# Optimization experiments

Measured on AMD Instinct MI355X. Metric: run time of the kernel, lower is better.

Reference implementation:

```python
import jax, jax.numpy as jnp
import numpy as np
from jax.ops import segment_sum

N = 100000
E = 1600000
NFEAT, NHID, NCLS = 128, 64, 40


def setup_inputs() -> dict:
    key = jax.random.key(0)
    ks = jax.random.split(key, 8)
    x = jax.random.normal(ks[0], (N, NFEAT), dtype=jnp.float32)
    edge_index = jax.random.randint(ks[1], (2, E), 0, N, dtype=jnp.int64)
    s = lambda fi, fo: (2.0 / (fi + fo)) ** 0.5  # glorot-ish
    W1 = jax.random.normal(ks[2], (NFEAT, NHID), dtype=jnp.float32) * s(NFEAT, NHID)
    b1 = jnp.zeros((NHID,), dtype=jnp.float32)
    W2 = jax.random.normal(ks[3], (NHID, NHID), dtype=jnp.float32) * s(NHID, NHID)
    b2 = jnp.zeros((NHID,), dtype=jnp.float32)
    Wc = jax.random.normal(ks[4], (NHID, NCLS), dtype=jnp.float32) * s(NHID, NCLS)
    bc = jnp.zeros((NCLS,), dtype=jnp.float32)
    return {"x": x, "edge_index": edge_index, "W1": W1, "b1": b1,
            "W2": W2, "b2": b2, "Wc": Wc, "bc": bc}


def _gcn_conv(x, W, b, row, col, dinv):
    # x: [N, Fin] -> [N, Fout]; symmetric-normalized aggregation (PyG GCNConv)
    h = x @ W                                   # [N, Fout]
    norm = dinv[row] * dinv[col]                # [E+N]
    msg = h[row] * norm[:, None]                # [E+N, Fout]
    out = segment_sum(msg, col, num_segments=N) # [N, Fout]
    return out + b


def reference(x, edge_index, W1, b1, W2, b2, Wc, bc):
    # add self loops
    loops = jnp.arange(N, dtype=edge_index.dtype)
    row = jnp.concatenate([edge_index[0], loops])
    col = jnp.concatenate([edge_index[1], loops])
    # symmetric normalization degrees (edge weight = 1)
    deg = segment_sum(jnp.ones_like(col, dtype=x.dtype), col, num_segments=N)
    dinv = jnp.where(deg > 0, jax.lax.rsqrt(deg), 0.0)
    h = jax.nn.relu(_gcn_conv(x, W1, b1, row, col, dinv))
    h = jax.nn.relu(_gcn_conv(h, W2, b2, row, col, dinv))
    return h @ Wc + bc
```

## Files before the change

### kernel.cpp

```cpp
#include <hip/hip_runtime.h>

#define NN 100000
#define NE 1600000
#define NF 128
#define NH 64
#define NC 40

#define BKN 128
#define NBK ((NN + BKN - 1) / BKN)
#define CH  4096
#define NCHB ((NE + CH - 1) / CH)
#define CAPB 2560
#define OFFS (BKN + 1)
#define HCAP 1408
#define HTS 36
#define XTS 68

typedef short bf16x8 __attribute__((ext_vector_type(8)));
typedef float f32x4  __attribute__((ext_vector_type(4)));

__device__ __forceinline__ unsigned short f2bf(float f) {
    unsigned int u = __builtin_bit_cast(unsigned int, f);
    u += 0x7FFFu + ((u >> 16) & 1u);
    return (unsigned short)(u >> 16);
}
__device__ __forceinline__ float bfl(unsigned int u) {
    return __builtin_bit_cast(float, u << 16);
}
__device__ __forceinline__ float bfh(unsigned int u) {
    return __builtin_bit_cast(float, u & 0xFFFF0000u);
}
__device__ __forceinline__ unsigned int pk2(float a, float b) {
    return (unsigned int)f2bf(a) | ((unsigned int)f2bf(b) << 16);
}
__device__ __forceinline__ void bacc8(float4& lo, float4& hi, uint4 v) {
    lo.x += bfl(v.x); hi.x += bfh(v.x);
    lo.y += bfl(v.y); hi.y += bfh(v.y);
    lo.z += bfl(v.z); hi.z += bfh(v.z);
    lo.w += bfl(v.w); hi.w += bfh(v.w);
}

__global__ __launch_bounds__(256) void prep_wt(const float* __restrict__ W1,
                                               const float* __restrict__ W2,
                                               const float* __restrict__ Wc,
                                               unsigned short* __restrict__ Wt1,
                                               unsigned short* __restrict__ Wt2,
                                               unsigned short* __restrict__ Wtc,
                                               int* __restrict__ gcnt) {
    int t = blockIdx.x * 256 + threadIdx.x;
    if (t < 8192) {
        int j = t >> 7, k = t & 127;
        Wt1[j * 128 + k] = f2bf(W1[k * 64 + j]);
    } else if (t < 8192 + 4096) {
        int u = t - 8192;
        int j = u >> 6, k = u & 63;
        Wt2[j * 64 + k] = f2bf(W2[k * 64 + j]);
    } else if (t < 8192 + 4096 + 3072) {
        int u = t - 8192 - 4096;
        int j = u >> 6, k = u & 63;
        Wtc[j * 64 + k] = (j < NC) ? f2bf(Wc[k * NC + j]) : (unsigned short)0;
    } else if (t < 8192 + 4096 + 3072 + NBK) {
        gcnt[t - 8192 - 4096 - 3072] = 0;
    }
}

__global__ __launch_bounds__(256) void bucket_scatter(const int* __restrict__ row,
                                                      const int* __restrict__ col,
                                                      int* __restrict__ gcnt,
                                                      unsigned int* __restrict__ encs) {
    __shared__ int h[NBK];
    __shared__ int loff[NBK];
    __shared__ int cur[NBK];
    __shared__ int gbase[NBK];
    __shared__ unsigned int stage[CH];
    __shared__ unsigned short sbkt[CH];
    int tid = threadIdx.x;
    for (int i = tid; i < NBK; i += 256) h[i] = 0;
    __syncthreads();
    int e0 = blockIdx.x * CH;
    int nval = NE - e0; if (nval > CH) nval = CH;
    int c[16];
    #pragma unroll
    for (int i = 0; i < 16; ++i) {
        int e = e0 + i * 256 + tid;
        c[i] = (e < NE) ? col[e] : -1;
        if (c[i] >= 0) atomicAdd(&h[c[i] >> 7], 1);
    }
    __syncthreads();
    if (tid < 64) {
        int lane = tid, base = lane * 13;
        int pre[13]; int sum = 0;
        #pragma unroll
        for (int j = 0; j < 13; ++j) {
            int idx = base + j;
            int x = (idx < NBK) ? h[idx] : 0;
            pre[j] = sum; sum += x;
        }
        int run = sum;
        #pragma unroll
        for (int d = 1; d < 64; d <<= 1) {
            int n = __shfl_up(run, d, 64);
            if (lane >= d) run += n;
        }
        int lex = run - sum;
        #pragma unroll
        for (int j = 0; j < 13; ++j) {
            int idx = base + j;
            if (idx < NBK) { loff[idx] = lex + pre[j]; cur[idx] = lex + pre[j]; }
        }
    }
    __syncthreads();
    for (int i = tid; i < NBK; i += 256) {
        int cnt = h[i];
        gbase[i] = cnt ? atomicAdd(&gcnt[i], cnt) : 0;
    }
    __syncthreads();
    #pragma unroll
    for (int i = 0; i < 16; ++i) {
        int e = e0 + i * 256 + tid;
        if (e < NE) {
            int cc = c[i], b = cc >> 7;
            int r = atomicAdd(&cur[b], 1);
            stage[r] = ((unsigned int)(cc & 127) << 24) | (unsigned int)row[e];
            sbkt[r] = (unsigned short)b;
        }
    }
    __syncthreads();
    for (int s = tid; s < nval; s += 256) {
        int b = sbkt[s];
        encs[(size_t)b * CAPB + gbase[b] + (s - loff[b])] = stage[s];
    }
}

__global__ __launch_bounds__(256) void csr_sort(unsigned int* __restrict__ encs,
                                                const int* __restrict__ gcnt,
                                                int* __restrict__ offg,
                                                float* __restrict__ dinv) {
    __shared__ unsigned int sseg[CAPB];
    __shared__ int h[BKN];
    __shared__ int off[OFFS];
    __shared__ int cur[BKN];
    int b = blockIdx.x, tid = threadIdx.x;
    if (tid < BKN) h[tid] = 0;
    __syncthreads();
    int m = gcnt[b];
    unsigned int* seg = encs + (size_t)b * CAPB;
    for (int s = tid; s < m; s += 256) {
        unsigned int e = seg[s];
        sseg[s] = e;
        atomicAdd(&h[e >> 24], 1);
    }
    __syncthreads();
    if (tid < BKN) {
        int g = b * BKN + tid;
        if (g < NN) dinv[g] = rsqrtf((float)(h[tid] + 1));
    }
    if (tid < 64) {
        int lane = tid;
        int x0 = h[lane * 2], x1 = h[lane * 2 + 1];
        int sum = x0 + x1, run = sum;
        #pragma unroll
        for (int d = 1; d < 64; d <<= 1) {
            int n = __shfl_up(run, d, 64);
            if (lane >= d) run += n;
        }
        int ex = run - sum;
        off[lane * 2] = ex;          cur[lane * 2] = ex;
        off[lane * 2 + 1] = ex + x0; cur[lane * 2 + 1] = ex + x0;
        if (lane == 63) off[BKN] = run;
    }
    __syncthreads();
    for (int s = tid; s < m; s += 256) {
        unsigned int e = sseg[s];
        int n = e >> 24;
        int r = atomicAdd(&cur[n], 1);
        seg[r] = e & 0xFFFFFFu;
    }
    if (tid < OFFS) offg[b * OFFS + tid] = off[tid];
}

__global__ __launch_bounds__(256) void gemm1_mfma(const float* __restrict__ x,
                                                  const unsigned short* __restrict__ Wt1,
                                                  const float* __restrict__ dinv,
                                                  unsigned short* __restrict__ hsb) {
    __shared__ unsigned int Xl[64 * XTS];
    __shared__ float sdv[64];
    int tid = threadIdx.x;
    int rbase = blockIdx.x * 64;
    if (tid < 64) {
        int r = rbase + tid;
        sdv[tid] = (r < NN) ? dinv[r] : 0.f;
    }
    #pragma unroll
    for (int p = 0; p < 8; ++p) {
        int fid = p * 256 + tid;
        int m = fid >> 5, c4 = fid & 31;
        int rr = rbase + m; if (rr >= NN) rr = NN - 1;
        float4 v = *(const float4*)(x + (size_t)rr * NF + c4 * 4);
        uint2 u;
        u.x = pk2(v.x, v.y);
        u.y = pk2(v.z, v.w);
        *(uint2*)&Xl[m * XTS + c4 * 2] = u;
    }
    __syncthreads();

    int wid = tid >> 6, lane = tid & 63;
    int lm = lane & 15, lg = lane >> 4;
    int rt = wid;
    bf16x8 af[4];
    #pragma unroll
    for (int kh = 0; kh < 4; ++kh)
        af[kh] = __builtin_bit_cast(bf16x8,
                    *(const uint4*)&Xl[(rt * 16 + lm) * XTS + kh * 16 + lg * 4]);
    f32x4 acc[4];
    #pragma unroll
    for (int ct = 0; ct < 4; ++ct) {
        acc[ct] = (f32x4){0.f, 0.f, 0.f, 0.f};
        #pragma unroll
        for (int kh = 0; kh < 4; ++kh) {
            bf16x8 bf = __builtin_bit_cast(bf16x8,
                *(const uint4*)(Wt1 + (size_t)(ct * 16 + lm) * 128 + kh * 32 + lg * 8));
            acc[ct] = __builtin_amdgcn_mfma_f32_16x16x32_bf16(af[kh], bf, acc[ct], 0, 0, 0);
        }
    }
    #pragma unroll
    for (int ct = 0; ct < 4; ++ct) {
        #pragma unroll
        for (int rg = 0; rg < 4; ++rg) {
            int rloc = rt * 16 + lg * 4 + rg;
            int r = rbase + rloc;
            if (r < NN)
                hsb[(size_t)r * NH + ct * 16 + lm] = f2bf(acc[ct][rg] * sdv[rloc]);
        }
    }
}

template <int FINAL>
__global__ __launch_bounds__(512) void agg_matmul(const unsigned short* __restrict__ hs,
                                                  const int* __restrict__ srow,
                                                  const int* __restrict__ offg,
                                                  const float* __restrict__ dinv,
                                                  const float* __restrict__ biasA,
                                                  const unsigned short* __restrict__ Wt,
                                                  const float* __restrict__ biasB,
                                                  unsigned short* __restrict__ hsb_out,
                                                  float* __restrict__ f_out) {
    __shared__ int off[65];
    __shared__ int sidx[HCAP];
    __shared__ unsigned int htb[64 * HTS];
    __shared__ float sdinv[64];
    int b = blockIdx.x >> 1, half = blockIdx.x & 1;
    int tid = threadIdx.x;
    int rbase = b * BKN + half * 64;
    if (tid < 65) off[tid] = offg[b * OFFS + half * 64 + tid];
    __syncthreads();
    int e0 = off[0], cnt = off[64] - e0;
    const int* ptr = srow + (size_t)b * CAPB + e0;
    for (int s = tid; s < cnt; s += 512) sidx[s] = ptr[s];
    __syncthreads();

    int n = tid >> 3, sl = tid & 7;
    int g = rbase + n;
    const uint4* hs8 = (const uint4*)hs;
    {
        float d = (g < NN) ? dinv[g] : 0.f;
        if (sl == 0) sdinv[n] = d;
        float4 o0 = {}, o1 = {};
        if (g < NN) {
            float4 lo0 = {}, hi0 = {}, lo1 = {}, hi1 = {};
            float4 lo2 = {}, hi2 = {}, lo3 = {}, hi3 = {};
            bacc8(lo0, hi0, hs8[(size_t)g * 8 + sl]);
            int e = off[n] - e0, ee = off[n + 1] - e0;
            for (; e + 8 <= ee; e += 8) {
                int r0 = sidx[e + 0], r1 = sidx[e + 1];
                int r2 = sidx[e + 2], r3 = sidx[e + 3];
                int r4 = sidx[e + 4], r5 = sidx[e + 5];
                int r6 = sidx[e + 6], r7 = sidx[e + 7];
                uint4 v0 = hs8[(size_t)r0 * 8 + sl];
                uint4 v1 = hs8[(size_t)r1 * 8 + sl];
                uint4 v2 = hs8[(size_t)r2 * 8 + sl];
                uint4 v3 = hs8[(size_t)r3 * 8 + sl];
                uint4 v4 = hs8[(size_t)r4 * 8 + sl];
                uint4 v5 = hs8[(size_t)r5 * 8 + sl];
                uint4 v6 = hs8[(size_t)r6 * 8 + sl];
                uint4 v7 = hs8[(size_t)r7 * 8 + sl];
                bacc8(lo0, hi0, v0); bacc8(lo1, hi1, v1);
                bacc8(lo2, hi2, v2); bacc8(lo3, hi3, v3);
                bacc8(lo0, hi0, v4); bacc8(lo1, hi1, v5);
                bacc8(lo2, hi2, v6); bacc8(lo3, hi3, v7);
            }
            if (e + 4 <= ee) {
                int r0 = sidx[e + 0], r1 = sidx[e + 1];
                int r2 = sidx[e + 2], r3 = sidx[e + 3];
                uint4 v0 = hs8[(size_t)r0 * 8 + sl];
                uint4 v1 = hs8[(size_t)r1 * 8 + sl];
                uint4 v2 = hs8[(size_t)r2 * 8 + sl];
                uint4 v3 = hs8[(size_t)r3 * 8 + sl];
                bacc8(lo0, hi0, v0); bacc8(lo1, hi1, v1);
                bacc8(lo2, hi2, v2); bacc8(lo3, hi3, v3);
                e += 4;
            }
            for (; e < ee; ++e)
                bacc8(lo0, hi0, hs8[(size_t)sidx[e] * 8 + sl]);
            lo0.x += lo1.x + lo2.x + lo3.x;  hi0.x += hi1.x + hi2.x + hi3.x;
            lo0.y += lo1.y + lo2.y + lo3.y;  hi0.y += hi1.y + hi2.y + hi3.y;
            lo0.z += lo1.z + lo2.z + lo3.z;  hi0.z += hi1.z + hi2.z + hi3.z;
            lo0.w += lo1.w + lo2.w + lo3.w;  hi0.w += hi1.w + hi2.w + hi3.w;
            float4 bb0 = ((const float4*)biasA)[sl * 2];
            float4 bb1 = ((const float4*)biasA)[sl * 2 + 1];
            o0.x = fmaxf(fmaf(lo0.x, d, bb0.x), 0.f);
            o0.y = fmaxf(fmaf(hi0.x, d, bb0.y), 0.f);
            o0.z = fmaxf(fmaf(lo0.y, d, bb0.z), 0.f);
            o0.w = fmaxf(fmaf(hi0.y, d, bb0.w), 0.f);
            o1.x = fmaxf(fmaf(lo0.z, d, bb1.x), 0.f);
            o1.y = fmaxf(fmaf(hi0.z, d, bb1.y), 0.f);
            o1.z = fmaxf(fmaf(lo0.w, d, bb1.z), 0.f);
            o1.w = fmaxf(fmaf(hi0.w, d, bb1.w), 0.f);
        }
        uint4 pk;
        pk.x = pk2(o0.x, o0.y);
        pk.y = pk2(o0.z, o0.w);
        pk.z = pk2(o1.x, o1.y);
        pk.w = pk2(o1.z, o1.w);
        *(uint4*)&htb[n * HTS + sl * 4] = pk;
    }
    __syncthreads();

    constexpr int NCT = FINAL ? 3 : 4;
    int wid = tid >> 6, lane = tid & 63;
    int lm = lane & 15, lg = lane >> 4;
    int rt = wid >> 1;
    int ct0 = (wid & 1) * 2;
    int ct1 = (ct0 + 2 < NCT) ? ct0 + 2 : NCT;
    bf16x8 afrag[2];
    #pragma unroll
    for (int kh = 0; kh < 2; ++kh) {
        const unsigned int* p = &htb[(rt * 16 + lm) * HTS + kh * 16 + lg * 4];
        afrag[kh] = __builtin_bit_cast(bf16x8, *(const uint4*)p);
    }
    for (int ct = ct0; ct < ct1; ++ct) {
        f32x4 acc = (f32x4){0.f, 0.f, 0.f, 0.f};
        #pragma unroll
        for (int kh = 0; kh < 2; ++kh) {
            const unsigned short* q = Wt + (size_t)(ct * 16 + lm) * 64 + kh * 32 + lg * 8;
            bf16x8 bfrag = __builtin_bit_cast(bf16x8, *(const uint4*)q);
            acc = __builtin_amdgcn_mfma_f32_16x16x32_bf16(afrag[kh], bfrag, acc, 0, 0, 0);
        }
        if (!FINAL) {
            #pragma unroll
            for (int rg = 0; rg < 4; ++rg) {
                int rloc = rt * 16 + lg * 4 + rg;
                int r = rbase + rloc;
                if (r < NN) {
                    float v = acc[rg] * sdinv[rloc];
                    hsb_out[(size_t)r * NH + ct * 16 + lm] = f2bf(v);
                }
            }
        } else {
            int c = ct * 16 + lm;
            if (c < NC) {
                float bb = biasB[c];
                #pragma unroll
                for (int rg = 0; rg < 4; ++rg) {
                    int rloc = rt * 16 + lg * 4 + rg;
                    int r = rbase + rloc;
                    if (r < NN)
                        f_out[(size_t)r * NC + c] = acc[rg] + bb;
                }
            }
        }
    }
}


extern "C" void kernel_launch(void* const* d_in, const int* in_sizes, int n_in,
                              void* d_out, int out_size, void* d_ws, size_t ws_size,
                              hipStream_t stream) {
    const float* x  = (const float*)d_in[0];
    const int* ei   = (const int*)d_in[1];
    const int* row  = ei;
    const int* col  = ei + NE;
    const float* W1 = (const float*)d_in[2];
    const float* b1 = (const float*)d_in[3];
    const float* W2 = (const float*)d_in[4];
    const float* b2 = (const float*)d_in[5];
    const float* Wc = (const float*)d_in[6];
    const float* bc = (const float*)d_in[7];
    float* out = (float*)d_out;

    char* ws = (char*)d_ws;
    size_t off = 0;
    auto alloc = [&](size_t bytes) {
        void* p = ws + off;
        off = (off + bytes + 255) & ~(size_t)255;
        return p;
    };
    int*   gcnt = (int*)alloc((size_t)NBK * 4);
    int*   offg = (int*)alloc((size_t)NBK * OFFS * 4);
    float* dinv = (float*)alloc((size_t)NN * 4);
    unsigned int* encs = (unsigned int*)alloc((size_t)NBK * CAPB * 4);
    unsigned short* hsb1 = (unsigned short*)alloc((size_t)NN * NH * 2);
    unsigned short* hsb2 = (unsigned short*)alloc((size_t)NN * NH * 2);
    unsigned short* Wt1  = (unsigned short*)alloc((size_t)64 * 128 * 2);
    unsigned short* Wt2  = (unsigned short*)alloc((size_t)64 * 64 * 2);
    unsigned short* Wtc  = (unsigned short*)alloc((size_t)48 * 64 * 2);

    const int GB = (NN + 63) / 64;

    prep_wt<<<64, 256, 0, stream>>>(W1, W2, Wc, Wt1, Wt2, Wtc, gcnt);
    bucket_scatter<<<NCHB, 256, 0, stream>>>(row, col, gcnt, encs);
    csr_sort<<<NBK, 256, 0, stream>>>(encs, gcnt, offg, dinv);

    gemm1_mfma<<<GB, 256, 0, stream>>>(x, Wt1, dinv, hsb1);
    agg_matmul<0><<<NBK * 2, 512, 0, stream>>>(hsb1, (const int*)encs, offg, dinv,
                                               b1, Wt2, nullptr, hsb2, nullptr);
    agg_matmul<1><<<NBK * 2, 512, 0, stream>>>(hsb2, (const int*)encs, offg, dinv,
                                               b2, Wtc, bc, nullptr, out);
}
```

Baseline: 151.3 us.

## Split features into plane-major slices with XCC-aware dynamic block scheduling

Hidden activations are stored as 8 feature planes of 8 bf16 values each. Aggregation is split per (bucket, plane), and blocks take work from atomic counters keyed by their XCC ID, so each XCC's L2 tends to serve one plane's gather working set. The fused aggregate+matmul kernels are split into a separate aggregation kernel and a plane-reading MFMA GEMM, which adds two launches and extra intermediate round-trips through memory. Each edge gather now fetches only 16 bytes, so there are more, smaller requests, in exchange for a smaller per-XCC L2 footprint.

```diff
diff --git a/kernel.cpp b/kernel.cpp
--- a/kernel.cpp
+++ b/kernel.cpp
@@ -12,8 +12,6 @@
 #define NCHB ((NE + CH - 1) / CH)
 #define CAPB 2560
 #define OFFS (BKN + 1)
-#define HCAP 1408
-#define HTS 36
 #define XTS 68
 
 typedef short bf16x8 __attribute__((ext_vector_type(8)));
@@ -33,11 +31,9 @@
 __device__ __forceinline__ unsigned int pk2(float a, float b) {
     return (unsigned int)f2bf(a) | ((unsigned int)f2bf(b) << 16);
 }
-__device__ __forceinline__ void bacc8(float4& lo, float4& hi, uint4 v) {
-    lo.x += bfl(v.x); hi.x += bfh(v.x);
-    lo.y += bfl(v.y); hi.y += bfh(v.y);
-    lo.z += bfl(v.z); hi.z += bfh(v.z);
-    lo.w += bfl(v.w); hi.w += bfh(v.w);
+__device__ __forceinline__ void add4(float4& a, uint2 v) {
+    a.x += bfl(v.x); a.y += bfh(v.x);
+    a.z += bfl(v.y); a.w += bfh(v.y);
 }
 
 __global__ __launch_bounds__(256) void prep_wt(const float* __restrict__ W1,
@@ -46,7 +42,8 @@
                                                unsigned short* __restrict__ Wt1,
                                                unsigned short* __restrict__ Wt2,
                                                unsigned short* __restrict__ Wtc,
-                                               int* __restrict__ gcnt) {
+                                               int* __restrict__ gcnt,
+                                               int* __restrict__ curs) {
     int t = blockIdx.x * 256 + threadIdx.x;
     if (t < 8192) {
         int j = t >> 7, k = t & 127;
@@ -59,8 +56,10 @@
         int u = t - 8192 - 4096;
         int j = u >> 6, k = u & 63;
         Wtc[j * 64 + k] = (j < NC) ? f2bf(Wc[k * NC + j]) : (unsigned short)0;
-    } else if (t < 8192 + 4096 + 3072 + NBK) {
-        gcnt[t - 8192 - 4096 - 3072] = 0;
+    } else if (t < 15360 + NBK) {
+        gcnt[t - 15360] = 0;
+    } else if (t < 15360 + NBK + 16) {
+        curs[t - 15360 - NBK] = 0;
     }
 }
 
@@ -182,7 +181,7 @@
 __global__ __launch_bounds__(256) void gemm1_mfma(const float* __restrict__ x,
                                                   const unsigned short* __restrict__ Wt1,
                                                   const float* __restrict__ dinv,
-                                                  unsigned short* __restrict__ hsb) {
+                                                  uint4* __restrict__ hsbT) {
     __shared__ unsigned int Xl[64 * XTS];
     __shared__ float sdv[64];
     int tid = threadIdx.x;
@@ -206,12 +205,11 @@
 
     int wid = tid >> 6, lane = tid & 63;
     int lm = lane & 15, lg = lane >> 4;
-    int rt = wid;
     bf16x8 af[4];
     #pragma unroll
     for (int kh = 0; kh < 4; ++kh)
         af[kh] = __builtin_bit_cast(bf16x8,
-                    *(const uint4*)&Xl[(rt * 16 + lm) * XTS + kh * 16 + lg * 4]);
+                    *(const uint4*)&Xl[(wid * 16 + lm) * XTS + kh * 16 + lg * 4]);
     f32x4 acc[4];
     #pragma unroll
     for (int ct = 0; ct < 4; ++ct) {
@@ -223,153 +221,156 @@
             acc[ct] = __builtin_amdgcn_mfma_f32_16x16x32_bf16(af[kh], bf, acc[ct], 0, 0, 0);
         }
     }
-    #pragma unroll
-    for (int ct = 0; ct < 4; ++ct) {
+    __syncthreads();
+    unsigned short* ot = (unsigned short*)Xl;
+    #pragma unroll
+    for (int ct = 0; ct < 4; ++ct)
         #pragma unroll
         for (int rg = 0; rg < 4; ++rg) {
-            int rloc = rt * 16 + lg * 4 + rg;
-            int r = rbase + rloc;
-            if (r < NN)
-                hsb[(size_t)r * NH + ct * 16 + lm] = f2bf(acc[ct][rg] * sdv[rloc]);
-        }
+            int rloc = wid * 16 + lg * 4 + rg;
+            ot[rloc * 72 + ct * 16 + lm] = f2bf(acc[ct][rg] * sdv[rloc]);
+        }
+    __syncthreads();
+    unsigned int* otU = (unsigned int*)Xl;
+    for (int j = tid; j < 512; j += 256) {
+        int p = j >> 6, i = j & 63;
+        int r = rbase + i;
+        if (r < NN)
+            hsbT[(size_t)p * NN + r] = *(uint4*)&otU[i * 36 + p * 4];
     }
 }
 
 template <int FINAL>
-__global__ __launch_bounds__(512) void agg_matmul(const unsigned short* __restrict__ hs,
-                                                  const int* __restrict__ srow,
-                                                  const int* __restrict__ offg,
-                                                  const float* __restrict__ dinv,
-                                                  const float* __restrict__ biasA,
-                                                  const unsigned short* __restrict__ Wt,
-                                                  const float* __restrict__ biasB,
-                                                  unsigned short* __restrict__ hsb_out,
-                                                  float* __restrict__ f_out) {
-    __shared__ int off[65];
-    __shared__ int sidx[HCAP];
-    __shared__ unsigned int htb[64 * HTS];
-    __shared__ float sdinv[64];
-    int b = blockIdx.x >> 1, half = blockIdx.x & 1;
-    int tid = threadIdx.x;
-    int rbase = b * BKN + half * 64;
-    if (tid < 65) off[tid] = offg[b * OFFS + half * 64 + tid];
-    __syncthreads();
-    int e0 = off[0], cnt = off[64] - e0;
-    const int* ptr = srow + (size_t)b * CAPB + e0;
-    for (int s = tid; s < cnt; s += 512) sidx[s] = ptr[s];
-    __syncthreads();
-
-    int n = tid >> 3, sl = tid & 7;
-    int g = rbase + n;
-    const uint4* hs8 = (const uint4*)hs;
-    {
-        float d = (g < NN) ? dinv[g] : 0.f;
-        if (sl == 0) sdinv[n] = d;
-        float4 o0 = {}, o1 = {};
-        if (g < NN) {
-            float4 lo0 = {}, hi0 = {}, lo1 = {}, hi1 = {};
-            float4 lo2 = {}, hi2 = {}, lo3 = {}, hi3 = {};
-            bacc8(lo0, hi0, hs8[(size_t)g * 8 + sl]);
-            int e = off[n] - e0, ee = off[n + 1] - e0;
-            for (; e + 8 <= ee; e += 8) {
-                int r0 = sidx[e + 0], r1 = sidx[e + 1];
-                int r2 = sidx[e + 2], r3 = sidx[e + 3];
-                int r4 = sidx[e + 4], r5 = sidx[e + 5];
-                int r6 = sidx[e + 6], r7 = sidx[e + 7];
-                uint4 v0 = hs8[(size_t)r0 * 8 + sl];
-                uint4 v1 = hs8[(size_t)r1 * 8 + sl];
-                uint4 v2 = hs8[(size_t)r2 * 8 + sl];
-                uint4 v3 = hs8[(size_t)r3 * 8 + sl];
-                uint4 v4 = hs8[(size_t)r4 * 8 + sl];
-                uint4 v5 = hs8[(size_t)r5 * 8 + sl];
-                uint4 v6 = hs8[(size_t)r6 * 8 + sl];
-                uint4 v7 = hs8[(size_t)r7 * 8 + sl];
-                bacc8(lo0, hi0, v0); bacc8(lo1, hi1, v1);
-                bacc8(lo2, hi2, v2); bacc8(lo3, hi3, v3);
-                bacc8(lo0, hi0, v4); bacc8(lo1, hi1, v5);
-                bacc8(lo2, hi2, v6); bacc8(lo3, hi3, v7);
-            }
-            if (e + 4 <= ee) {
-                int r0 = sidx[e + 0], r1 = sidx[e + 1];
-                int r2 = sidx[e + 2], r3 = sidx[e + 3];
-                uint4 v0 = hs8[(size_t)r0 * 8 + sl];
-                uint4 v1 = hs8[(size_t)r1 * 8 + sl];
-                uint4 v2 = hs8[(size_t)r2 * 8 + sl];
-                uint4 v3 = hs8[(size_t)r3 * 8 + sl];
-                bacc8(lo0, hi0, v0); bacc8(lo1, hi1, v1);
-                bacc8(lo2, hi2, v2); bacc8(lo3, hi3, v3);
-                e += 4;
-            }
-            for (; e < ee; ++e)
-                bacc8(lo0, hi0, hs8[(size_t)sidx[e] * 8 + sl]);
-            lo0.x += lo1.x + lo2.x + lo3.x;  hi0.x += hi1.x + hi2.x + hi3.x;
-            lo0.y += lo1.y + lo2.y + lo3.y;  hi0.y += hi1.y + hi2.y + hi3.y;
-            lo0.z += lo1.z + lo2.z + lo3.z;  hi0.z += hi1.z + hi2.z + hi3.z;
-            lo0.w += lo1.w + lo2.w + lo3.w;  hi0.w += hi1.w + hi2.w + hi3.w;
-            float4 bb0 = ((const float4*)biasA)[sl * 2];
-            float4 bb1 = ((const float4*)biasA)[sl * 2 + 1];
-            o0.x = fmaxf(fmaf(lo0.x, d, bb0.x), 0.f);
-            o0.y = fmaxf(fmaf(hi0.x, d, bb0.y), 0.f);
-            o0.z = fmaxf(fmaf(lo0.y, d, bb0.z), 0.f);
-            o0.w = fmaxf(fmaf(hi0.y, d, bb0.w), 0.f);
-            o1.x = fmaxf(fmaf(lo0.z, d, bb1.x), 0.f);
-            o1.y = fmaxf(fmaf(hi0.z, d, bb1.y), 0.f);
-            o1.z = fmaxf(fmaf(lo0.w, d, bb1.z), 0.f);
-            o1.w = fmaxf(fmaf(hi0.w, d, bb1.w), 0.f);
-        }
-        uint4 pk;
-        pk.x = pk2(o0.x, o0.y);
-        pk.y = pk2(o0.z, o0.w);
-        pk.z = pk2(o1.x, o1.y);
-        pk.w = pk2(o1.z, o1.w);
-        *(uint4*)&htb[n * HTS + sl * 4] = pk;
-    }
-    __syncthreads();
-
-    constexpr int NCT = FINAL ? 3 : 4;
+__global__ __launch_bounds__(256) void gemm_planes(const uint4* __restrict__ hT,
+                                                   const unsigned short* __restrict__ Wt,
+                                                   const float* __restrict__ dinv,
+                                                   const float* __restrict__ biasB,
+                                                   uint4* __restrict__ hsbT_out,
+                                                   float* __restrict__ f_out) {
+    __shared__ unsigned int ot[64 * 36 + 16];
+    int tid = threadIdx.x, rbase = blockIdx.x * 64;
     int wid = tid >> 6, lane = tid & 63;
     int lm = lane & 15, lg = lane >> 4;
-    int rt = wid >> 1;
-    int ct0 = (wid & 1) * 2;
-    int ct1 = (ct0 + 2 < NCT) ? ct0 + 2 : NCT;
-    bf16x8 afrag[2];
+    int arow = rbase + wid * 16 + lm; if (arow >= NN) arow = NN - 1;
+    bf16x8 af[2];
     #pragma unroll
     for (int kh = 0; kh < 2; ++kh) {
-        const unsigned int* p = &htb[(rt * 16 + lm) * HTS + kh * 16 + lg * 4];
-        afrag[kh] = __builtin_bit_cast(bf16x8, *(const uint4*)p);
-    }
-    for (int ct = ct0; ct < ct1; ++ct) {
-        f32x4 acc = (f32x4){0.f, 0.f, 0.f, 0.f};
+        int p = kh * 4 + lg;
+        af[kh] = __builtin_bit_cast(bf16x8, hT[(size_t)p * NN + arow]);
+    }
+    constexpr int NCT = FINAL ? 3 : 4;
+    f32x4 acc[NCT];
+    #pragma unroll
+    for (int ct = 0; ct < NCT; ++ct) {
+        acc[ct] = (f32x4){0.f, 0.f, 0.f, 0.f};
         #pragma unroll
         for (int kh = 0; kh < 2; ++kh) {
-            const unsigned short* q = Wt + (size_t)(ct * 16 + lm) * 64 + kh * 32 + lg * 8;
-            bf16x8 bfrag = __builtin_bit_cast(bf16x8, *(const uint4*)q);
-            acc = __builtin_amdgcn_mfma_f32_16x16x32_bf16(afrag[kh], bfrag, acc, 0, 0, 0);
-        }
-        if (!FINAL) {
+            bf16x8 bf = __builtin_bit_cast(bf16x8,
+                *(const uint4*)(Wt + (size_t)(ct * 16 + lm) * 64 + kh * 32 + lg * 8));
+            acc[ct] = __builtin_amdgcn_mfma_f32_16x16x32_bf16(af[kh], bf, acc[ct], 0, 0, 0);
+        }
+    }
+
+    if (!FINAL) {
+        unsigned short* ots = (unsigned short*)ot;
+        #pragma unroll
+        for (int ct = 0; ct < NCT; ++ct)
             #pragma unroll
             for (int rg = 0; rg < 4; ++rg) {
-                int rloc = rt * 16 + lg * 4 + rg;
+                int rloc = wid * 16 + lg * 4 + rg;
                 int r = rbase + rloc;
-                if (r < NN) {
-                    float v = acc[rg] * sdinv[rloc];
-                    hsb_out[(size_t)r * NH + ct * 16 + lm] = f2bf(v);
-                }
+                float d = (r < NN) ? dinv[r] : 0.f;
+                ots[rloc * 72 + ct * 16 + lm] = f2bf(acc[ct][rg] * d);
             }
-        } else {
+        __syncthreads();
+        for (int j = tid; j < 512; j += 256) {
+            int p = j >> 6, i = j & 63;
+            int r = rbase + i;
+            if (r < NN)
+                hsbT_out[(size_t)p * NN + r] = *(uint4*)&ot[i * 36 + p * 4];
+        }
+    } else {
+        #pragma unroll
+        for (int ct = 0; ct < NCT; ++ct) {
             int c = ct * 16 + lm;
             if (c < NC) {
                 float bb = biasB[c];
                 #pragma unroll
                 for (int rg = 0; rg < 4; ++rg) {
-                    int rloc = rt * 16 + lg * 4 + rg;
-                    int r = rbase + rloc;
+                    int r = rbase + wid * 16 + lg * 4 + rg;
                     if (r < NN)
-                        f_out[(size_t)r * NC + c] = acc[rg] + bb;
+                        f_out[(size_t)r * NC + c] = acc[ct][rg] + bb;
                 }
             }
         }
     }
+}
+
+__global__ __launch_bounds__(256) void agg_sliced(const uint2* __restrict__ hsbT,
+                                                  const unsigned int* __restrict__ encs,
+                                                  const int* __restrict__ offg,
+                                                  const float* __restrict__ dinv,
+                                                  const float* __restrict__ biasA,
+                                                  uint2* __restrict__ hT_out,
+                                                  int* __restrict__ curs) {
+    __shared__ int sbq;
+    int tid = threadIdx.x;
+    if (tid == 0) {
+        int xcc;
+        asm volatile("s_getreg_b32 %0, hwreg(HW_REG_XCC_ID)" : "=s"(xcc));
+        int q0 = xcc & 7, q = q0, b = NBK;
+        #pragma unroll 1
+        for (int t = 0; t < 8; ++t) {
+            q = (q0 + t) & 7;
+            b = atomicAdd(&curs[q], 1);
+            if (b < NBK) break;
+        }
+        sbq = (b < NBK) ? (b * 8 + q) : -1;
+    }
+    __syncthreads();
+    int bq = sbq;
+    if (bq < 0) return;
+    int b = bq >> 3, q = bq & 7;
+    int team = tid >> 1, l = tid & 1;
+    int g = b * BKN + team;
+    if (g >= NN) return;
+    const uint2* pl = hsbT + (size_t)q * NN * 2;
+    int e  = offg[b * OFFS + team];
+    int ee = offg[b * OFFS + team + 1];
+    const unsigned int* sp = encs + (size_t)b * CAPB;
+    float4 A0 = {}, A1 = {};
+    add4(A0, pl[(size_t)g * 2 + l]);
+    for (; e + 8 <= ee; e += 8) {
+        int r0 = sp[e + 0], r1 = sp[e + 1], r2 = sp[e + 2], r3 = sp[e + 3];
+        int r4 = sp[e + 4], r5 = sp[e + 5], r6 = sp[e + 6], r7 = sp[e + 7];
+        uint2 v0 = pl[(size_t)r0 * 2 + l], v1 = pl[(size_t)r1 * 2 + l];
+        uint2 v2 = pl[(size_t)r2 * 2 + l], v3 = pl[(size_t)r3 * 2 + l];
+        uint2 v4 = pl[(size_t)r4 * 2 + l], v5 = pl[(size_t)r5 * 2 + l];
+        uint2 v6 = pl[(size_t)r6 * 2 + l], v7 = pl[(size_t)r7 * 2 + l];
+        add4(A0, v0); add4(A1, v1); add4(A0, v2); add4(A1, v3);
+        add4(A0, v4); add4(A1, v5); add4(A0, v6); add4(A1, v7);
+    }
+    if (e + 4 <= ee) {
+        int r0 = sp[e + 0], r1 = sp[e + 1], r2 = sp[e + 2], r3 = sp[e + 3];
+        uint2 v0 = pl[(size_t)r0 * 2 + l], v1 = pl[(size_t)r1 * 2 + l];
+        uint2 v2 = pl[(size_t)r2 * 2 + l], v3 = pl[(size_t)r3 * 2 + l];
+        add4(A0, v0); add4(A1, v1); add4(A0, v2); add4(A1, v3);
+        e += 4;
+    }
+    for (; e < ee; ++e)
+        add4(A0, pl[(size_t)sp[e] * 2 + l]);
+    A0.x += A1.x; A0.y += A1.y; A0.z += A1.z; A0.w += A1.w;
+    float d = dinv[g];
+    float4 bb = *(const float4*)(biasA + q * 8 + l * 4);
+    float4 o;
+    o.x = fmaxf(fmaf(A0.x, d, bb.x), 0.f);
+    o.y = fmaxf(fmaf(A0.y, d, bb.y), 0.f);
+    o.z = fmaxf(fmaf(A0.z, d, bb.z), 0.f);
+    o.w = fmaxf(fmaf(A0.w, d, bb.w), 0.f);
+    uint2 pkv;
+    pkv.x = pk2(o.x, o.y);
+    pkv.y = pk2(o.z, o.w);
+    hT_out[((size_t)q * NN + g) * 2 + l] = pkv;
 }
 
 
@@ -396,24 +397,29 @@
         return p;
     };
     int*   gcnt = (int*)alloc((size_t)NBK * 4);
+    int*   curs = (int*)alloc(64);
     int*   offg = (int*)alloc((size_t)NBK * OFFS * 4);
     float* dinv = (float*)alloc((size_t)NN * 4);
     unsigned int* encs = (unsigned int*)alloc((size_t)NBK * CAPB * 4);
-    unsigned short* hsb1 = (unsigned short*)alloc((size_t)NN * NH * 2);
-    unsigned short* hsb2 = (unsigned short*)alloc((size_t)NN * NH * 2);
-    unsigned short* Wt1  = (unsigned short*)alloc((size_t)64 * 128 * 2);
-    unsigned short* Wt2  = (unsigned short*)alloc((size_t)64 * 64 * 2);
-    unsigned short* Wtc  = (unsigned short*)alloc((size_t)48 * 64 * 2);
+    uint4* hsbT1 = (uint4*)alloc((size_t)NN * NH * 2);
+    uint4* hsbT2 = (uint4*)alloc((size_t)NN * NH * 2);
+    uint4* h1T   = (uint4*)alloc((size_t)NN * NH * 2);
+    uint4* h2T   = (uint4*)alloc((size_t)NN * NH * 2);
+    unsigned short* Wt1 = (unsigned short*)alloc((size_t)64 * 128 * 2);
+    unsigned short* Wt2 = (unsigned short*)alloc((size_t)64 * 64 * 2);
+    unsigned short* Wtc = (unsigned short*)alloc((size_t)48 * 64 * 2);
 
     const int GB = (NN + 63) / 64;
 
-    prep_wt<<<64, 256, 0, stream>>>(W1, W2, Wc, Wt1, Wt2, Wtc, gcnt);
+    prep_wt<<<64, 256, 0, stream>>>(W1, W2, Wc, Wt1, Wt2, Wtc, gcnt, curs);
     bucket_scatter<<<NCHB, 256, 0, stream>>>(row, col, gcnt, encs);
     csr_sort<<<NBK, 256, 0, stream>>>(encs, gcnt, offg, dinv);
 
-    gemm1_mfma<<<GB, 256, 0, stream>>>(x, Wt1, dinv, hsb1);
-    agg_matmul<0><<<NBK * 2, 512, 0, stream>>>(hsb1, (const int*)encs, offg, dinv,
-                                               b1, Wt2, nullptr, hsb2, nullptr);
-    agg_matmul<1><<<NBK * 2, 512, 0, stream>>>(hsb2, (const int*)encs, offg, dinv,
-                                               b2, Wtc, bc, nullptr, out);
-}
+    gemm1_mfma<<<GB, 256, 0, stream>>>(x, Wt1, dinv, hsbT1);
+    agg_sliced<<<NBK * 8, 256, 0, stream>>>((const uint2*)hsbT1, encs, offg, dinv,
+                                            b1, (uint2*)h1T, curs);
+    gemm_planes<0><<<GB, 256, 0, stream>>>(h1T, Wt2, dinv, nullptr, hsbT2, nullptr);
+    agg_sliced<<<NBK * 8, 256, 0, stream>>>((const uint2*)hsbT2, encs, offg, dinv,
+                                            b2, (uint2*)h2T, curs + 8);
+    gemm_planes<1><<<GB, 256, 0, stream>>>(h2T, Wtc, nullptr, bc, nullptr, out);
+}
```

Result: slower. 290.8 us (+92.2%).

## Split fused aggregation+matmul into separate aggregation and row-GEMM kernels

Applied to the files above, without the earlier changes.

Replaces the fused agg_matmul kernel with an agg_bucket kernel, which writes the bias+ReLU aggregated bf16 features to global memory. A separate gemm_rows MFMA kernel then applies the next weight matrix. The aggregation kernel uses 256 threads per block, each processing two nodes, and no longer holds the shared tile, which may improve occupancy for the gather-bound phase. The cost is an extra global round trip of the intermediate table and two additional kernel launches per forward pass.

```diff
diff --git a/kernel.cpp b/kernel.cpp
--- a/kernel.cpp
+++ b/kernel.cpp
@@ -13,7 +13,6 @@
 #define CAPB 2560
 #define OFFS (BKN + 1)
 #define HCAP 1408
-#define HTS 36
 #define XTS 68
 
 typedef short bf16x8 __attribute__((ext_vector_type(8)));
@@ -206,12 +205,11 @@
 
     int wid = tid >> 6, lane = tid & 63;
     int lm = lane & 15, lg = lane >> 4;
-    int rt = wid;
     bf16x8 af[4];
     #pragma unroll
     for (int kh = 0; kh < 4; ++kh)
         af[kh] = __builtin_bit_cast(bf16x8,
-                    *(const uint4*)&Xl[(rt * 16 + lm) * XTS + kh * 16 + lg * 4]);
+                    *(const uint4*)&Xl[(wid * 16 + lm) * XTS + kh * 16 + lg * 4]);
     f32x4 acc[4];
     #pragma unroll
     for (int ct = 0; ct < 4; ++ct) {
@@ -227,7 +225,7 @@
     for (int ct = 0; ct < 4; ++ct) {
         #pragma unroll
         for (int rg = 0; rg < 4; ++rg) {
-            int rloc = rt * 16 + lg * 4 + rg;
+            int rloc = wid * 16 + lg * 4 + rg;
             int r = rbase + rloc;
             if (r < NN)
                 hsb[(size_t)r * NH + ct * 16 + lm] = f2bf(acc[ct][rg] * sdv[rloc]);
@@ -235,37 +233,30 @@
     }
 }
 
-template <int FINAL>
-__global__ __launch_bounds__(512) void agg_matmul(const unsigned short* __restrict__ hs,
+__global__ __launch_bounds__(256) void agg_bucket(const unsigned short* __restrict__ hs,
                                                   const int* __restrict__ srow,
                                                   const int* __restrict__ offg,
                                                   const float* __restrict__ dinv,
-                                                  const float* __restrict__ biasA,
-                                                  const unsigned short* __restrict__ Wt,
-                                                  const float* __restrict__ biasB,
-                                                  unsigned short* __restrict__ hsb_out,
-                                                  float* __restrict__ f_out) {
+                                                  const float* __restrict__ bias,
+                                                  unsigned short* __restrict__ hb_out) {
     __shared__ int off[65];
     __shared__ int sidx[HCAP];
-    __shared__ unsigned int htb[64 * HTS];
-    __shared__ float sdinv[64];
     int b = blockIdx.x >> 1, half = blockIdx.x & 1;
     int tid = threadIdx.x;
-    int rbase = b * BKN + half * 64;
     if (tid < 65) off[tid] = offg[b * OFFS + half * 64 + tid];
     __syncthreads();
     int e0 = off[0], cnt = off[64] - e0;
     const int* ptr = srow + (size_t)b * CAPB + e0;
-    for (int s = tid; s < cnt; s += 512) sidx[s] = ptr[s];
-    __syncthreads();
-
-    int n = tid >> 3, sl = tid & 7;
-    int g = rbase + n;
+    for (int s = tid; s < cnt; s += 256) sidx[s] = ptr[s];
+    __syncthreads();
+
+    int wid = tid >> 6, lane = tid & 63;
+    int sg = lane >> 3, sl = lane & 7;
     const uint4* hs8 = (const uint4*)hs;
-    {
-        float d = (g < NN) ? dinv[g] : 0.f;
-        if (sl == 0) sdinv[n] = d;
-        float4 o0 = {}, o1 = {};
+    #pragma unroll
+    for (int k = 0; k < 2; ++k) {
+        int n = k * 32 + wid * 8 + sg;
+        int g = b * BKN + half * 64 + n;
         if (g < NN) {
             float4 lo0 = {}, hi0 = {}, lo1 = {}, hi1 = {};
             float4 lo2 = {}, hi2 = {}, lo3 = {}, hi3 = {};
@@ -306,8 +297,10 @@
             lo0.y += lo1.y + lo2.y + lo3.y;  hi0.y += hi1.y + hi2.y + hi3.y;
             lo0.z += lo1.z + lo2.z + lo3.z;  hi0.z += hi1.z + hi2.z + hi3.z;
             lo0.w += lo1.w + lo2.w + lo3.w;  hi0.w += hi1.w + hi2.w + hi3.w;
-            float4 bb0 = ((const float4*)biasA)[sl * 2];
-            float4 bb1 = ((const float4*)biasA)[sl * 2 + 1];
+            float d = dinv[g];
+            float4 bb0 = ((const float4*)bias)[sl * 2];
+            float4 bb1 = ((const float4*)bias)[sl * 2 + 1];
+            float4 o0, o1;
             o0.x = fmaxf(fmaf(lo0.x, d, bb0.x), 0.f);
             o0.y = fmaxf(fmaf(hi0.x, d, bb0.y), 0.f);
             o0.z = fmaxf(fmaf(lo0.y, d, bb0.z), 0.f);
@@ -316,45 +309,60 @@
             o1.y = fmaxf(fmaf(hi0.z, d, bb1.y), 0.f);
             o1.z = fmaxf(fmaf(lo0.w, d, bb1.z), 0.f);
             o1.w = fmaxf(fmaf(hi0.w, d, bb1.w), 0.f);
-        }
-        uint4 pk;
-        pk.x = pk2(o0.x, o0.y);
-        pk.y = pk2(o0.z, o0.w);
-        pk.z = pk2(o1.x, o1.y);
-        pk.w = pk2(o1.z, o1.w);
-        *(uint4*)&htb[n * HTS + sl * 4] = pk;
-    }
-    __syncthreads();
-
-    constexpr int NCT = FINAL ? 3 : 4;
+            uint4 pk;
+            pk.x = pk2(o0.x, o0.y);
+            pk.y = pk2(o0.z, o0.w);
+            pk.z = pk2(o1.x, o1.y);
+            pk.w = pk2(o1.z, o1.w);
+            ((uint4*)hb_out)[(size_t)g * 8 + sl] = pk;
+        }
+    }
+}
+
+template <int FINAL>
+__global__ __launch_bounds__(256) void gemm_rows(const unsigned short* __restrict__ hb,
+                                                 const unsigned short* __restrict__ Wt,
+                                                 const float* __restrict__ dinv,
+                                                 const float* __restrict__ biasB,
+                                                 unsigned short* __restrict__ hsb_out,
+                                                 float* __restrict__ f_out) {
+    __shared__ float sdv[64];
+    int tid = threadIdx.x;
+    int rbase = blockIdx.x * 64;
+    if (!FINAL && tid < 64) {
+        int r = rbase + tid;
+        sdv[tid] = (r < NN) ? dinv[r] : 0.f;
+    }
     int wid = tid >> 6, lane = tid & 63;
     int lm = lane & 15, lg = lane >> 4;
-    int rt = wid >> 1;
-    int ct0 = (wid & 1) * 2;
-    int ct1 = (ct0 + 2 < NCT) ? ct0 + 2 : NCT;
-    bf16x8 afrag[2];
-    #pragma unroll
-    for (int kh = 0; kh < 2; ++kh) {
-        const unsigned int* p = &htb[(rt * 16 + lm) * HTS + kh * 16 + lg * 4];
-        afrag[kh] = __builtin_bit_cast(bf16x8, *(const uint4*)p);
-    }
-    for (int ct = ct0; ct < ct1; ++ct) {
-        f32x4 acc = (f32x4){0.f, 0.f, 0.f, 0.f};
+    int ra = rbase + wid * 16 + lm; if (ra >= NN) ra = NN - 1;
+    bf16x8 af[2];
+    #pragma unroll
+    for (int kh = 0; kh < 2; ++kh)
+        af[kh] = __builtin_bit_cast(bf16x8,
+                    ((const uint4*)hb)[(size_t)ra * 8 + kh * 4 + lg]);
+    constexpr int NCT = FINAL ? 3 : 4;
+    f32x4 acc[NCT];
+    #pragma unroll
+    for (int ct = 0; ct < NCT; ++ct) {
+        acc[ct] = (f32x4){0.f, 0.f, 0.f, 0.f};
         #pragma unroll
         for (int kh = 0; kh < 2; ++kh) {
-            const unsigned short* q = Wt + (size_t)(ct * 16 + lm) * 64 + kh * 32 + lg * 8;
-            bf16x8 bfrag = __builtin_bit_cast(bf16x8, *(const uint4*)q);
-            acc = __builtin_amdgcn_mfma_f32_16x16x32_bf16(afrag[kh], bfrag, acc, 0, 0, 0);
-        }
+            bf16x8 bf = __builtin_bit_cast(bf16x8,
+                *(const uint4*)(Wt + (size_t)(ct * 16 + lm) * 64 + kh * 32 + lg * 8));
+            acc[ct] = __builtin_amdgcn_mfma_f32_16x16x32_bf16(af[kh], bf, acc[ct], 0, 0, 0);
+        }
+    }
+    if (!FINAL) __syncthreads();
+    #pragma unroll
+    for (int ct = 0; ct < NCT; ++ct) {
         if (!FINAL) {
             #pragma unroll
             for (int rg = 0; rg < 4; ++rg) {
-                int rloc = rt * 16 + lg * 4 + rg;
+                int rloc = wid * 16 + lg * 4 + rg;
                 int r = rbase + rloc;
-                if (r < NN) {
-                    float v = acc[rg] * sdinv[rloc];
-                    hsb_out[(size_t)r * NH + ct * 16 + lm] = f2bf(v);
-                }
+                if (r < NN)
+                    hsb_out[(size_t)r * NH + ct * 16 + lm] = f2bf(acc[ct][rg] * sdv[rloc]);
             }
         } else {
             int c = ct * 16 + lm;
@@ -362,10 +370,9 @@
                 float bb = biasB[c];
                 #pragma unroll
                 for (int rg = 0; rg < 4; ++rg) {
-                    int rloc = rt * 16 + lg * 4 + rg;
-                    int r = rbase + rloc;
+                    int r = rbase + wid * 16 + lg * 4 + rg;
                     if (r < NN)
-                        f_out[(size_t)r * NC + c] = acc[rg] + bb;
+                        f_out[(size_t)r * NC + c] = acc[ct][rg] + bb;
                 }
             }
         }
@@ -399,8 +406,8 @@
     int*   offg = (int*)alloc((size_t)NBK * OFFS * 4);
     float* dinv = (float*)alloc((size_t)NN * 4);
     unsigned int* encs = (unsigned int*)alloc((size_t)NBK * CAPB * 4);
-    unsigned short* hsb1 = (unsigned short*)alloc((size_t)NN * NH * 2);
-    unsigned short* hsb2 = (unsigned short*)alloc((size_t)NN * NH * 2);
+    unsigned short* tabA = (unsigned short*)alloc((size_t)NN * NH * 2);
+    unsigned short* tabB = (unsigned short*)alloc((size_t)NN * NH * 2);
     unsigned short* Wt1  = (unsigned short*)alloc((size_t)64 * 128 * 2);
     unsigned short* Wt2  = (unsigned short*)alloc((size_t)64 * 64 * 2);
     unsigned short* Wtc  = (unsigned short*)alloc((size_t)48 * 64 * 2);
@@ -411,9 +418,9 @@
     bucket_scatter<<<NCHB, 256, 0, stream>>>(row, col, gcnt, encs);
     csr_sort<<<NBK, 256, 0, stream>>>(encs, gcnt, offg, dinv);
 
-    gemm1_mfma<<<GB, 256, 0, stream>>>(x, Wt1, dinv, hsb1);
-    agg_matmul<0><<<NBK * 2, 512, 0, stream>>>(hsb1, (const int*)encs, offg, dinv,
-                                               b1, Wt2, nullptr, hsb2, nullptr);
-    agg_matmul<1><<<NBK * 2, 512, 0, stream>>>(hsb2, (const int*)encs, offg, dinv,
-                                               b2, Wtc, bc, nullptr, out);
-}
+    gemm1_mfma<<<GB, 256, 0, stream>>>(x, Wt1, dinv, tabA);
+    agg_bucket<<<NBK * 2, 256, 0, stream>>>(tabA, (const int*)encs, offg, dinv, b1, tabB);
+    gemm_rows<0><<<GB, 256, 0, stream>>>(tabB, Wt2, dinv, nullptr, tabA, nullptr);
+    agg_bucket<<<NBK * 2, 256, 0, stream>>>(tabA, (const int*)encs, offg, dinv, b2, tabB);
+    gemm_rows<1><<<GB, 256, 0, stream>>>(tabB, Wtc, nullptr, bc, nullptr, out);
+}
```

Result: slower. 157.0 us (+3.8%).
